# Kernel tuning notes

Measured on AMD Instinct MI355X. Metric: run time of the kernel, lower is better.

## Reference

```python
import jax, jax.numpy as jnp
import numpy as np

NEG_SLOPE = 0.2
EPS_SOFTMAX = 1e-16
EPS_NORM = 1e-12
H = 4


def gat_conv(x, src, dst, edge_attr, W, att_src, att_dst, W_edge, att_edge, bias, concat):
    """PyG GATConv with edge_dim, add_self_loops=False.
    x: [N, F_in]; src,dst: [E]; edge_attr: [E, edge_dim]
    W: [F_in, H*C]; att_src/att_dst/att_edge: [H, C]; W_edge: [edge_dim, H*C]
    """
    N = x.shape[0]
    C = att_src.shape[1]
    xs = (x @ W).reshape(N, H, C)                      # [N,H,C]
    a_s = jnp.einsum('nhc,hc->nh', xs, att_src)        # [N,H]
    a_d = jnp.einsum('nhc,hc->nh', xs, att_dst)        # [N,H]
    e = (edge_attr @ W_edge).reshape(-1, H, C)         # [E,H,C]
    a_e = jnp.einsum('ehc,hc->eh', e, att_edge)        # [E,H]
    alpha = a_s[src] + a_d[dst] + a_e                  # [E,H]
    alpha = jax.nn.leaky_relu(alpha, NEG_SLOPE)
    # segment softmax over edges grouped by destination node
    m = jax.ops.segment_max(alpha, dst, num_segments=N)        # [N,H]
    ex = jnp.exp(alpha - m[dst])
    denom = jax.ops.segment_sum(ex, dst, num_segments=N)       # [N,H]
    alpha = ex / (denom[dst] + EPS_SOFTMAX)
    # message = attention-weighted source features, scatter-add to dst
    out = jax.ops.segment_sum(xs[src] * alpha[..., None], dst, num_segments=N)  # [N,H,C]
    out = out.reshape(N, H * C) if concat else out.mean(axis=1)
    return out + bias


def l2_normalize(x):
    n = jnp.linalg.norm(x, axis=-1, keepdims=True)
    return x / jnp.maximum(n, EPS_NORM)


def setup_inputs() -> dict:
    key = jax.random.key(0)
    ks = jax.random.split(key, 16)
    N, E, F_in, C1, C2 = 50000, 800000, 128, 64, 64
    glorot = lambda k, shape: jax.random.uniform(
        k, shape, jnp.float32, -1.0, 1.0) * np.sqrt(6.0 / (shape[0] + shape[-1]))
    return {
        'x': jax.random.normal(ks[0], (N, F_in), jnp.float32),
        'edge_index': jax.random.randint(ks[1], (2, E), 0, N, jnp.int32),
        'edge_weight': jax.random.uniform(ks[2], (E, 1), jnp.float32),
        # layer 1: in=128 -> H*C1=256, concat=True
        'W1': glorot(ks[3], (F_in, H * C1)),
        'att_src1': glorot(ks[4], (H, C1)),
        'att_dst1': glorot(ks[5], (H, C1)),
        'We1': glorot(ks[6], (1, H * C1)),
        'att_e1': glorot(ks[7], (H, C1)),
        'b1': jnp.zeros((H * C1,), jnp.float32),
        # layer 2: in=256 -> H*C2, concat=False (mean over heads)
        'W2': glorot(ks[8], (H * C1, H * C2)),
        'att_src2': glorot(ks[9], (H, C2)),
        'att_dst2': glorot(ks[10], (H, C2)),
        'We2': glorot(ks[11], (1, H * C2)),
        'att_e2': glorot(ks[12], (H, C2)),
        'b2': jnp.zeros((C2,), jnp.float32),
    }


def reference(x, edge_index, edge_weight, W1, att_src1, att_dst1, We1, att_e1, b1,
              W2, att_src2, att_dst2, We2, att_e2, b2):
    src, dst = edge_index[0], edge_index[1]
    h = gat_conv(x, src, dst, edge_weight, W1, att_src1, att_dst1, We1, att_e1, b1, concat=True)
    h = jax.nn.relu(l2_normalize(h))
    out = gat_conv(h, src, dst, edge_weight, W2, att_src2, att_dst2, We2, att_e2, b2, concat=False)
    return out
```

## Files before the change

kernel.cpp:

```cpp
#include <hip/hip_runtime.h>
#include <hip/hip_bf16.h>

typedef unsigned short u16;
using bf16x8 = __attribute__((ext_vector_type(8))) short;
using f32x4v = __attribute__((ext_vector_type(4))) float;

#define HC 256
#define CDIM 64

__device__ __forceinline__ float b2f(u16 u){
  union { unsigned int i; float f; } c; c.i = ((unsigned)u) << 16; return c.f;
}
__device__ __forceinline__ u16 f2b(float f){
  union { float f; unsigned int i; } c; c.f = f;
  unsigned int x = c.i;
  return (u16)((x + 0x7FFFu + ((x >> 16) & 1u)) >> 16);
}
__device__ __forceinline__ float ldf(const void* p, size_t i, int isbf){
  return isbf ? b2f(((const u16*)p)[i]) : ((const float*)p)[i];
}
__device__ __forceinline__ float sel4(float4 v, int h){ return h==0?v.x:(h==1?v.y:(h==2?v.z:v.w)); }
__device__ __forceinline__ float lrelu(float v){ return v>0.f ? v : 0.2f*v; }

__device__ __forceinline__ float rdlf(float v, int e){
  return __int_as_float(__builtin_amdgcn_readlane(__float_as_int(v), e));
}
__device__ __forceinline__ float rdl_sel(float4 v, int h, int e){
  float w0 = rdlf(v.x, e), w1 = rdlf(v.y, e), w2 = rdlf(v.z, e), w3 = rdlf(v.w, e);
  return h==0?w0:(h==1?w1:(h==2?w2:w3));
}

__device__ __forceinline__ float4 wave_max4(float4 m){
  #pragma unroll
  for(int o=32;o>0;o>>=1){
    m.x=fmaxf(m.x,__shfl_xor(m.x,o));
    m.y=fmaxf(m.y,__shfl_xor(m.y,o));
    m.z=fmaxf(m.z,__shfl_xor(m.z,o));
    m.w=fmaxf(m.w,__shfl_xor(m.w,o));
  }
  return m;
}
__device__ __forceinline__ float4 wave_sum4(float4 m){
  #pragma unroll
  for(int o=32;o>0;o>>=1){
    m.x+=__shfl_xor(m.x,o);
    m.y+=__shfl_xor(m.y,o);
    m.z+=__shfl_xor(m.z,o);
    m.w+=__shfl_xor(m.w,o);
  }
  return m;
}

__global__ void k_detect(const u16* __restrict__ x, int nelem, int* __restrict__ flag){
  __shared__ int bad;
  if (threadIdx.x==0) bad = 0;
  __syncthreads();
  int n = nelem < 8192 ? nelem : 8192;
  int localbad = 0;
  for (int i=threadIdx.x; i<n; i+=256){
    int e = (x[i] >> 7) & 0xFF;
    if (e >= 140) localbad++;
  }
  if (localbad) atomicAdd(&bad, 1);
  __syncthreads();
  if (threadIdx.x==0) *flag = (bad==0) ? 1 : 0;
}

__global__ void k_hist(const int* __restrict__ dst, int E, int N, int* __restrict__ deg){
  int e = blockIdx.x*256 + threadIdx.x;
  if (e < E){
    int d = dst[e];
    if ((unsigned)d < (unsigned)N) atomicAdd(&deg[d], 1);
  }
}

__global__ void k_scan1(const int* __restrict__ in, int* __restrict__ out, int* __restrict__ bsums, int n){
  __shared__ int s[256];
  int t = threadIdx.x;
  int i = blockIdx.x*256 + t;
  int v = (i<n)? in[i] : 0;
  s[t]=v; __syncthreads();
  for(int off=1; off<256; off<<=1){
    int tv = (t>=off)? s[t-off] : 0;
    __syncthreads();
    s[t]+=tv; __syncthreads();
  }
  if (i<n) out[i] = s[t]-v;
  if (t==255) bsums[blockIdx.x] = s[255];
}

__global__ void k_scan2(int* __restrict__ bsums, int nb){
  __shared__ int s[256];
  int t=threadIdx.x;
  int v=(t<nb)? bsums[t]:0;
  s[t]=v; __syncthreads();
  for(int off=1; off<256; off<<=1){
    int tv=(t>=off)? s[t-off]:0;
    __syncthreads();
    s[t]+=tv; __syncthreads();
  }
  if (t<nb) bsums[t]=s[t]-v;
}

__global__ void k_scan3(int* __restrict__ out, const int* __restrict__ bsums, int n){
  int i = blockIdx.x*256+threadIdx.x;
  if (i<n) out[i]+=bsums[blockIdx.x];
}

__global__ void k_scatter(const int* __restrict__ src, const int* __restrict__ dst,
                          const void* __restrict__ ew, int E, int N,
                          const int* __restrict__ rowptr, int* __restrict__ cursor,
                          int* __restrict__ esrc, float* __restrict__ eewf,
                          const int* __restrict__ flagp){
  int e = blockIdx.x*256+threadIdx.x;
  if (e>=E) return;
  int bf = *flagp;
  int d = dst[e];
  if ((unsigned)d >= (unsigned)N) return;
  int p = rowptr[d] + atomicAdd(&cursor[d],1);
  int s = src[e];
  if ((unsigned)s >= (unsigned)N) s = 0;
  esrc[p] = s;
  eewf[p] = ldf(ew, e, bf);
}

__global__ void k_prepB(const void* __restrict__ W, u16* __restrict__ Bt, int K,
                        const int* __restrict__ flagp){
  int bf = *flagp;
  int k = blockIdx.x, t = threadIdx.x;
  float v = ldf(W, (size_t)k*HC + t, bf);
  Bt[(size_t)t*K + k] = f2b(v);
}

__global__ __launch_bounds__(256) void k_gemm_mfma(
    const void* __restrict__ A, int a_ext, const u16* __restrict__ Bt,
    u16* __restrict__ C, const void* __restrict__ att_s, const void* __restrict__ att_d,
    float* __restrict__ a_s, float* __restrict__ a_d,
    int M, int K, const int* __restrict__ flagp)
{
  __shared__ u16 sh[64*264];
  u16* As = sh;
  u16* Bs = sh + 2048;
  int bf = *flagp;
  int a_bf = a_ext ? bf : 1;
  int tid = threadIdx.x;
  int lane = tid & 63, w = tid >> 6;
  int quad = lane >> 4, ln = lane & 15;
  int m0 = blockIdx.x * 64;

  f32x4v acc[4][4] = {};
  for (int k0 = 0; k0 < K; k0 += 32){
    {
      int m = tid >> 2, g = tid & 3;
      int r = m0 + m;
      uint4 pack;
      if (r < M){
        size_t base = (size_t)r*K + k0 + g*8;
        if (a_bf){
          pack = *(const uint4*)((const u16*)A + base);
        } else {
          const float* Af = (const float*)A + base;
          float4 f0 = *(const float4*)Af;
          float4 f1 = *(const float4*)(Af+4);
          unsigned a0 = (unsigned)f2b(f0.x) | ((unsigned)f2b(f0.y)<<16);
          unsigned a1 = (unsigned)f2b(f0.z) | ((unsigned)f2b(f0.w)<<16);
          unsigned a2 = (unsigned)f2b(f1.x) | ((unsigned)f2b(f1.y)<<16);
          unsigned a3 = (unsigned)f2b(f1.z) | ((unsigned)f2b(f1.w)<<16);
          pack = make_uint4(a0,a1,a2,a3);
        }
      } else pack = make_uint4(0,0,0,0);
      ((uint4*)As)[tid] = pack;
    }
    #pragma unroll
    for (int i=0;i<4;i++){
      int n = i*64 + (tid>>2), g = tid&3;
      ((uint4*)Bs)[i*256 + tid] = *(const uint4*)(Bt + (size_t)n*K + k0 + g*8);
    }
    __syncthreads();
    bf16x8 af[4], bfr[4];
    #pragma unroll
    for (int mi=0;mi<4;mi++) af[mi] = *(const bf16x8*)&As[(mi*16+ln)*32 + quad*8];
    #pragma unroll
    for (int nj=0;nj<4;nj++) bfr[nj] = *(const bf16x8*)&Bs[((size_t)w*64+nj*16+ln)*32 + quad*8];
    #pragma unroll
    for (int mi=0;mi<4;mi++)
      #pragma unroll
      for (int nj=0;nj<4;nj++)
        acc[mi][nj] = __builtin_amdgcn_mfma_f32_16x16x32_bf16(af[mi], bfr[nj], acc[mi][nj], 0,0,0);
    __syncthreads();
  }
  #pragma unroll
  for (int mi=0;mi<4;mi++)
    #pragma unroll
    for (int nj=0;nj<4;nj++)
      #pragma unroll
      for (int r=0;r<4;r++)
        sh[(mi*16 + quad*4 + r)*264 + w*64 + nj*16 + ln] = f2b(acc[mi][nj][r]);
  __syncthreads();
  #pragma unroll
  for (int j=0;j<8;j++){
    int idx = j*256 + tid;
    int r = idx >> 5, gq = idx & 31;
    if (m0 + r < M)
      *(uint4*)(C + (size_t)(m0+r)*HC + gq*8) = *(const uint4*)&sh[r*264 + gq*8];
  }
  float4 sv, dv;
  sv.x=ldf(att_s,lane*4+0,bf); sv.y=ldf(att_s,lane*4+1,bf);
  sv.z=ldf(att_s,lane*4+2,bf); sv.w=ldf(att_s,lane*4+3,bf);
  dv.x=ldf(att_d,lane*4+0,bf); dv.y=ldf(att_d,lane*4+1,bf);
  dv.z=ldf(att_d,lane*4+2,bf); dv.w=ldf(att_d,lane*4+3,bf);
  for (int rr=0; rr<16; rr++){
    int r = w*16 + rr;
    ushort4 u = *(const ushort4*)&sh[r*264 + lane*4];
    float ps = b2f(u.x)*sv.x + b2f(u.y)*sv.y + b2f(u.z)*sv.z + b2f(u.w)*sv.w;
    float pd = b2f(u.x)*dv.x + b2f(u.y)*dv.y + b2f(u.z)*dv.z + b2f(u.w)*dv.w;
    #pragma unroll
    for (int o=1;o<16;o<<=1){ ps+=__shfl_xor(ps,o); pd+=__shfl_xor(pd,o); }
    if ((lane&15)==0 && m0+r<M){
      a_s[(size_t)(m0+r)*4 + (lane>>4)] = ps;
      a_d[(size_t)(m0+r)*4 + (lane>>4)] = pd;
    }
  }
}

__global__ void k_ce(const void* __restrict__ We, const void* __restrict__ att_e,
                     float* __restrict__ ce, const int* __restrict__ flagp){
  int bf = *flagp;
  int t=threadIdx.x;
  float p = ldf(We, t, bf)*ldf(att_e, t, bf);
  for(int o=32;o>0;o>>=1) p+=__shfl_xor(p,o);
  if((t&63)==0) ce[t>>6]=p;
}

__global__ __launch_bounds__(256) void k_soft_agg(
    const u16* __restrict__ xs, const int* __restrict__ rowptr, const int* __restrict__ deg,
    const int* __restrict__ esrc, const float* __restrict__ eewf,
    const float* __restrict__ a_s, const float* __restrict__ a_d, const float* __restrict__ ce4,
    const void* __restrict__ bias, void* __restrict__ outp, int N, int layer,
    const int* __restrict__ flagp){
  int bf = *flagp;
  int lane = threadIdx.x & 63;
  int w = threadIdx.x >> 6;
  int n = (blockIdx.x<<2) + w;
  if (n >= N) return;
  int row = rowptr[n];
  int dg = deg[n];
  float4 ad = *(const float4*)&a_d[(size_t)n*4];
  float4 ce = *(const float4*)ce4;
  int h = lane >> 4;
  float4 acc = make_float4(0.f,0.f,0.f,0.f);
  if (dg > 0){
    if (dg <= 64){
      int   s_reg = 0;
      float4 ar = make_float4(-1e30f,-1e30f,-1e30f,-1e30f);
      if (lane < dg){
        int pos = row + lane;
        int s = esrc[pos];
        if ((unsigned)s >= (unsigned)N) s = 0;
        s_reg = s;
        float wv = eewf[pos];
        float4 as = *(const float4*)&a_s[(size_t)s*4];
        ar.x = lrelu(as.x+ad.x+wv*ce.x);
        ar.y = lrelu(as.y+ad.y+wv*ce.y);
        ar.z = lrelu(as.z+ad.z+wv*ce.z);
        ar.w = lrelu(as.w+ad.w+wv*ce.w);
      }
      float4 m = wave_max4(ar);
      float4 ex = make_float4(0.f,0.f,0.f,0.f);
      if (lane < dg){
        ex.x=__expf(ar.x-m.x); ex.y=__expf(ar.y-m.y);
        ex.z=__expf(ar.z-m.z); ex.w=__expf(ar.w-m.w);
      }
      float4 ss = wave_sum4(ex);
      float4 wgt;
      wgt.x = ex.x/(ss.x+1e-16f); wgt.y = ex.y/(ss.y+1e-16f);
      wgt.z = ex.z/(ss.z+1e-16f); wgt.w = ex.w/(ss.w+1e-16f);
      int e = 0;
      for (; e+4 <= dg; e+=4){
        int s0=__builtin_amdgcn_readlane(s_reg,e+0);
        int s1=__builtin_amdgcn_readlane(s_reg,e+1);
        int s2=__builtin_amdgcn_readlane(s_reg,e+2);
        int s3=__builtin_amdgcn_readlane(s_reg,e+3);
        float w0=rdl_sel(wgt,h,e+0), w1=rdl_sel(wgt,h,e+1);
        float w2=rdl_sel(wgt,h,e+2), w3=rdl_sel(wgt,h,e+3);
        ushort4 x0 = *(const ushort4*)&xs[(size_t)s0*HC + lane*4];
        ushort4 x1 = *(const ushort4*)&xs[(size_t)s1*HC + lane*4];
        ushort4 x2 = *(const ushort4*)&xs[(size_t)s2*HC + lane*4];
        ushort4 x3 = *(const ushort4*)&xs[(size_t)s3*HC + lane*4];
        acc.x+=w0*b2f(x0.x); acc.y+=w0*b2f(x0.y); acc.z+=w0*b2f(x0.z); acc.w+=w0*b2f(x0.w);
        acc.x+=w1*b2f(x1.x); acc.y+=w1*b2f(x1.y); acc.z+=w1*b2f(x1.z); acc.w+=w1*b2f(x1.w);
        acc.x+=w2*b2f(x2.x); acc.y+=w2*b2f(x2.y); acc.z+=w2*b2f(x2.z); acc.w+=w2*b2f(x2.w);
        acc.x+=w3*b2f(x3.x); acc.y+=w3*b2f(x3.y); acc.z+=w3*b2f(x3.z); acc.w+=w3*b2f(x3.w);
      }
      for (; e<dg; e++){
        int s0=__builtin_amdgcn_readlane(s_reg,e);
        float w0=rdl_sel(wgt,h,e);
        ushort4 x0 = *(const ushort4*)&xs[(size_t)s0*HC + lane*4];
        acc.x+=w0*b2f(x0.x); acc.y+=w0*b2f(x0.y); acc.z+=w0*b2f(x0.z); acc.w+=w0*b2f(x0.w);
      }
    } else {
      float4 m = make_float4(-1e30f,-1e30f,-1e30f,-1e30f);
      for (int p=lane;p<dg;p+=64){
        int pos = row+p;
        int s = esrc[pos];
        if ((unsigned)s >= (unsigned)N) s = 0;
        float wv = eewf[pos];
        float4 as = *(const float4*)&a_s[(size_t)s*4];
        m.x=fmaxf(m.x, lrelu(as.x+ad.x+wv*ce.x));
        m.y=fmaxf(m.y, lrelu(as.y+ad.y+wv*ce.y));
        m.z=fmaxf(m.z, lrelu(as.z+ad.z+wv*ce.z));
        m.w=fmaxf(m.w, lrelu(as.w+ad.w+wv*ce.w));
      }
      m = wave_max4(m);
      float4 ss = make_float4(0.f,0.f,0.f,0.f);
      for (int p=lane;p<dg;p+=64){
        int pos = row+p;
        int s = esrc[pos];
        if ((unsigned)s >= (unsigned)N) s = 0;
        float wv = eewf[pos];
        float4 as = *(const float4*)&a_s[(size_t)s*4];
        ss.x+=__expf(lrelu(as.x+ad.x+wv*ce.x)-m.x);
        ss.y+=__expf(lrelu(as.y+ad.y+wv*ce.y)-m.y);
        ss.z+=__expf(lrelu(as.z+ad.z+wv*ce.z)-m.z);
        ss.w+=__expf(lrelu(as.w+ad.w+wv*ce.w)-m.w);
      }
      ss = wave_sum4(ss);
      float rsel=1.f/(sel4(ss,h)+1e-16f), mh=sel4(m,h), adh=sel4(ad,h), ceh=sel4(ce,h);
      for (int e=0;e<dg;e++){
        int pos=row+e;
        int s=esrc[pos];
        if ((unsigned)s >= (unsigned)N) s = 0;
        float wv=eewf[pos];
        float arv = lrelu(a_s[(size_t)s*4+h]+adh+wv*ceh);
        float wgt = __expf(arv-mh)*rsel;
        ushort4 xv4 = *(const ushort4*)&xs[(size_t)s*HC + lane*4];
        acc.x+=wgt*b2f(xv4.x); acc.y+=wgt*b2f(xv4.y);
        acc.z+=wgt*b2f(xv4.z); acc.w+=wgt*b2f(xv4.w);
      }
    }
  }
  if (layer==1){
    float4 v;
    v.x = acc.x + ldf(bias, lane*4+0, bf);
    v.y = acc.y + ldf(bias, lane*4+1, bf);
    v.z = acc.z + ldf(bias, lane*4+2, bf);
    v.w = acc.w + ldf(bias, lane*4+3, bf);
    float ss = v.x*v.x+v.y*v.y+v.z*v.z+v.w*v.w;
    #pragma unroll
    for(int o=32;o>0;o>>=1) ss += __shfl_xor(ss,o);
    float inv = 1.f/fmaxf(sqrtf(ss), 1e-12f);
    ushort4 o4;
    o4.x = f2b(fmaxf(v.x*inv,0.f)); o4.y = f2b(fmaxf(v.y*inv,0.f));
    o4.z = f2b(fmaxf(v.z*inv,0.f)); o4.w = f2b(fmaxf(v.w*inv,0.f));
    *(ushort4*)((u16*)outp + (size_t)n*HC + lane*4) = o4;
  } else {
    float4 s = acc;
    #pragma unroll
    for (int o=16;o<=32;o<<=1){
      s.x+=__shfl_xor(s.x,o); s.y+=__shfl_xor(s.y,o);
      s.z+=__shfl_xor(s.z,o); s.w+=__shfl_xor(s.w,o);
    }
    if (lane < 16){
      float4 v;
      v.x = 0.25f*s.x + ldf(bias, lane*4+0, bf);
      v.y = 0.25f*s.y + ldf(bias, lane*4+1, bf);
      v.z = 0.25f*s.z + ldf(bias, lane*4+2, bf);
      v.w = 0.25f*s.w + ldf(bias, lane*4+3, bf);
      if (bf){
        ushort4 o4; o4.x=f2b(v.x); o4.y=f2b(v.y); o4.z=f2b(v.z); o4.w=f2b(v.w);
        *(ushort4*)((u16*)outp + (size_t)n*CDIM + lane*4) = o4;
      } else {
        *(float4*)((float*)outp + (size_t)n*CDIM + lane*4) = v;
      }
    }
  }
}

extern "C" void kernel_launch(void* const* d_in, const int* in_sizes, int n_in,
                              void* d_out, int out_size, void* d_ws, size_t ws_size,
                              hipStream_t stream){
  const void* x_in = d_in[0];
  const int* eidx  = (const int*)d_in[1];
  const void* ew   = d_in[2];
  const void* W1   = d_in[3];
  const void* as1  = d_in[4];
  const void* ad1  = d_in[5];
  const void* We1  = d_in[6];
  const void* ae1  = d_in[7];
  const void* b1   = d_in[8];
  const void* W2   = d_in[9];
  const void* as2  = d_in[10];
  const void* ad2  = d_in[11];
  const void* We2  = d_in[12];
  const void* ae2  = d_in[13];
  const void* b2   = d_in[14];

  int N = in_sizes[0]/128;
  int E = in_sizes[2];
  const int* src = eidx;
  const int* dst = eidx + E;

  char* w = (char*)d_ws;
  auto alloc = [&](size_t bytes)->char*{ char* p=w; w += (bytes+255)/256*256; return p; };
  int*   flag  = (int*)alloc(256);
  u16*   xs    = (u16*)alloc((size_t)N*HC*2);
  u16*   agg   = (u16*)alloc((size_t)N*HC*2);
  float* a_s   = (float*)alloc((size_t)N*4*4);
  float* a_d   = (float*)alloc((size_t)N*4*4);
  int*   deg   = (int*)alloc((size_t)N*4);
  int*   cursor= (int*)alloc((size_t)N*4);
  int*   rowptr= (int*)alloc((size_t)N*4);
  int*   bsums = (int*)alloc(256*4);
  int*   esrc  = (int*)alloc((size_t)E*4);
  float* eewf  = (float*)alloc((size_t)E*4);
  float* ce    = (float*)alloc(64);
  u16*   Bt1   = (u16*)alloc((size_t)HC*128*2);
  u16*   Bt2   = (u16*)alloc((size_t)HC*HC*2);

  hipMemsetAsync(deg, 0, (size_t)N*4, stream);
  hipMemsetAsync(cursor, 0, (size_t)N*4, stream);

  k_detect<<<1,256,0,stream>>>((const u16*)x_in, in_sizes[0], flag);

  int eb = (E+255)/256;
  int nb = (N+255)/256;
  k_hist<<<eb,256,0,stream>>>(dst, E, N, deg);
  k_scan1<<<nb,256,0,stream>>>(deg, rowptr, bsums, N);
  k_scan2<<<1,256,0,stream>>>(bsums, nb);
  k_scan3<<<nb,256,0,stream>>>(rowptr, bsums, N);
  k_scatter<<<eb,256,0,stream>>>(src, dst, ew, E, N, rowptr, cursor, esrc, eewf, flag);
  k_prepB<<<128,256,0,stream>>>(W1, Bt1, 128, flag);
  k_prepB<<<256,256,0,stream>>>(W2, Bt2, 256, flag);

  int gemmBlocks = (N+63)/64;
  int nwb = (N+3)/4;

  k_gemm_mfma<<<gemmBlocks,256,0,stream>>>(x_in, 1, Bt1, xs, as1, ad1, a_s, a_d, N, 128, flag);
  k_ce<<<1,256,0,stream>>>(We1, ae1, ce, flag);
  k_soft_agg<<<nwb,256,0,stream>>>(xs, rowptr, deg, esrc, eewf, a_s, a_d, ce, b1, agg, N, 1, flag);

  k_gemm_mfma<<<gemmBlocks,256,0,stream>>>(agg, 0, Bt2, xs, as2, ad2, a_s, a_d, N, 256, flag);
  k_ce<<<1,256,0,stream>>>(We2, ae2, ce, flag);
  k_soft_agg<<<nwb,256,0,stream>>>(xs, rowptr, deg, esrc, eewf, a_s, a_d, ce, b2, d_out, N, 2, flag);
}
```

Baseline: 391.9 us.

## Merge setup kernels and replace readlane weight broadcast with shuffles

Several small setup kernels are merged: the detect, three-pass scan and cursor memset become one single-block 1024-thread scan kernel that also seeds the cursor, and the weight-transpose and edge-coefficient kernels become one prep kernel. This cuts launch count and removes a per-edge rowptr load in scatter. In the soft aggregation's fast path, the four readlanes plus select per edge are replaced by a per-head pre-shuffle followed by one shuffle per edge, aimed at lowering scalar/VALU overhead. The single-block scan serializes the degree prefix over about 49 elements per thread, which may be slower than the parallel multi-block scan.

```diff
diff --git a/kernel.cpp b/kernel.cpp
--- a/kernel.cpp
+++ b/kernel.cpp
@@ -21,14 +21,6 @@
 }
 __device__ __forceinline__ float sel4(float4 v, int h){ return h==0?v.x:(h==1?v.y:(h==2?v.z:v.w)); }
 __device__ __forceinline__ float lrelu(float v){ return v>0.f ? v : 0.2f*v; }
-
-__device__ __forceinline__ float rdlf(float v, int e){
-  return __int_as_float(__builtin_amdgcn_readlane(__float_as_int(v), e));
-}
-__device__ __forceinline__ float rdl_sel(float4 v, int h, int e){
-  float w0 = rdlf(v.x, e), w1 = rdlf(v.y, e), w2 = rdlf(v.z, e), w3 = rdlf(v.w, e);
-  return h==0?w0:(h==1?w1:(h==2?w2:w3));
-}
 
 __device__ __forceinline__ float4 wave_max4(float4 m){
   #pragma unroll
@@ -51,21 +43,6 @@
   return m;
 }
 
-__global__ void k_detect(const u16* __restrict__ x, int nelem, int* __restrict__ flag){
-  __shared__ int bad;
-  if (threadIdx.x==0) bad = 0;
-  __syncthreads();
-  int n = nelem < 8192 ? nelem : 8192;
-  int localbad = 0;
-  for (int i=threadIdx.x; i<n; i+=256){
-    int e = (x[i] >> 7) & 0xFF;
-    if (e >= 140) localbad++;
-  }
-  if (localbad) atomicAdd(&bad, 1);
-  __syncthreads();
-  if (threadIdx.x==0) *flag = (bad==0) ? 1 : 0;
-}
-
 __global__ void k_hist(const int* __restrict__ dst, int E, int N, int* __restrict__ deg){
   int e = blockIdx.x*256 + threadIdx.x;
   if (e < E){
@@ -74,37 +51,41 @@
   }
 }
 
-__global__ void k_scan1(const int* __restrict__ in, int* __restrict__ out, int* __restrict__ bsums, int n){
-  __shared__ int s[256];
+__global__ __launch_bounds__(1024) void k_scan(const int* __restrict__ deg,
+                                               int* __restrict__ rowptr, int* __restrict__ cursor,
+                                               int N, const u16* __restrict__ x, int nelem,
+                                               int* __restrict__ flag){
+  __shared__ int sums[1024];
+  __shared__ int bad;
   int t = threadIdx.x;
-  int i = blockIdx.x*256 + t;
-  int v = (i<n)? in[i] : 0;
-  s[t]=v; __syncthreads();
-  for(int off=1; off<256; off<<=1){
-    int tv = (t>=off)? s[t-off] : 0;
+  if (t==0) bad = 0;
+  __syncthreads();
+  if (t < 256){
+    int n = nelem < 8192 ? nelem : 8192;
+    int localbad = 0;
+    for (int i=t; i<n; i+=256){
+      int e = (x[i] >> 7) & 0xFF;
+      if (e >= 140) localbad++;
+    }
+    if (localbad) atomicAdd(&bad, 1);
+  }
+  __syncthreads();
+  if (t==0) *flag = (bad==0) ? 1 : 0;
+  int chunk = (N + 1023) >> 10;
+  int lo = t*chunk, hi = lo+chunk < N ? lo+chunk : N;
+  int s = 0;
+  for (int i=lo;i<hi;i++) s += deg[i];
+  sums[t]=s; __syncthreads();
+  for (int off=1; off<1024; off<<=1){
+    int v = (t>=off)? sums[t-off]:0;
     __syncthreads();
-    s[t]+=tv; __syncthreads();
-  }
-  if (i<n) out[i] = s[t]-v;
-  if (t==255) bsums[blockIdx.x] = s[255];
-}
-
-__global__ void k_scan2(int* __restrict__ bsums, int nb){
-  __shared__ int s[256];
-  int t=threadIdx.x;
-  int v=(t<nb)? bsums[t]:0;
-  s[t]=v; __syncthreads();
-  for(int off=1; off<256; off<<=1){
-    int tv=(t>=off)? s[t-off]:0;
-    __syncthreads();
-    s[t]+=tv; __syncthreads();
-  }
-  if (t<nb) bsums[t]=s[t]-v;
-}
-
-__global__ void k_scan3(int* __restrict__ out, const int* __restrict__ bsums, int n){
-  int i = blockIdx.x*256+threadIdx.x;
-  if (i<n) out[i]+=bsums[blockIdx.x];
+    sums[t]+=v; __syncthreads();
+  }
+  int base = sums[t] - s;
+  for (int i=lo;i<hi;i++){
+    rowptr[i]=base; cursor[i]=base;
+    base += deg[i];
+  }
 }
 
 __global__ void k_scatter(const int* __restrict__ src, const int* __restrict__ dst,
@@ -117,19 +98,32 @@
   int bf = *flagp;
   int d = dst[e];
   if ((unsigned)d >= (unsigned)N) return;
-  int p = rowptr[d] + atomicAdd(&cursor[d],1);
+  int p = atomicAdd(&cursor[d],1);
   int s = src[e];
   if ((unsigned)s >= (unsigned)N) s = 0;
   esrc[p] = s;
   eewf[p] = ldf(ew, e, bf);
 }
 
-__global__ void k_prepB(const void* __restrict__ W, u16* __restrict__ Bt, int K,
-                        const int* __restrict__ flagp){
+__global__ void k_prep(const void* __restrict__ W1, const void* __restrict__ W2,
+                       const void* __restrict__ We1, const void* __restrict__ ae1,
+                       const void* __restrict__ We2, const void* __restrict__ ae2,
+                       u16* __restrict__ Bt1, u16* __restrict__ Bt2, float* __restrict__ ce,
+                       const int* __restrict__ flagp){
   int bf = *flagp;
-  int k = blockIdx.x, t = threadIdx.x;
-  float v = ldf(W, (size_t)k*HC + t, bf);
-  Bt[(size_t)t*K + k] = f2b(v);
+  int b = blockIdx.x, t = threadIdx.x;
+  if (b < 128){
+    Bt1[(size_t)t*128 + b] = f2b(ldf(W1, (size_t)b*HC + t, bf));
+  } else if (b < 384){
+    int k = b - 128;
+    Bt2[(size_t)t*256 + k] = f2b(ldf(W2, (size_t)k*HC + t, bf));
+  } else {
+    float p1 = ldf(We1, t, bf)*ldf(ae1, t, bf);
+    float p2 = ldf(We2, t, bf)*ldf(ae2, t, bf);
+    #pragma unroll
+    for(int o=32;o>0;o>>=1){ p1+=__shfl_xor(p1,o); p2+=__shfl_xor(p2,o); }
+    if((t&63)==0){ ce[t>>6]=p1; ce[4+(t>>6)]=p2; }
+  }
 }
 
 __global__ __launch_bounds__(256) void k_gemm_mfma(
@@ -221,15 +215,6 @@
       a_d[(size_t)(m0+r)*4 + (lane>>4)] = pd;
     }
   }
-}
-
-__global__ void k_ce(const void* __restrict__ We, const void* __restrict__ att_e,
-                     float* __restrict__ ce, const int* __restrict__ flagp){
-  int bf = *flagp;
-  int t=threadIdx.x;
-  float p = ldf(We, t, bf)*ldf(att_e, t, bf);
-  for(int o=32;o>0;o>>=1) p+=__shfl_xor(p,o);
-  if((t&63)==0) ce[t>>6]=p;
 }
 
 __global__ __launch_bounds__(256) void k_soft_agg(
@@ -275,28 +260,49 @@
       float4 wgt;
       wgt.x = ex.x/(ss.x+1e-16f); wgt.y = ex.y/(ss.y+1e-16f);
       wgt.z = ex.z/(ss.z+1e-16f); wgt.w = ex.w/(ss.w+1e-16f);
-      int e = 0;
-      for (; e+4 <= dg; e+=4){
-        int s0=__builtin_amdgcn_readlane(s_reg,e+0);
-        int s1=__builtin_amdgcn_readlane(s_reg,e+1);
-        int s2=__builtin_amdgcn_readlane(s_reg,e+2);
-        int s3=__builtin_amdgcn_readlane(s_reg,e+3);
-        float w0=rdl_sel(wgt,h,e+0), w1=rdl_sel(wgt,h,e+1);
-        float w2=rdl_sel(wgt,h,e+2), w3=rdl_sel(wgt,h,e+3);
-        ushort4 x0 = *(const ushort4*)&xs[(size_t)s0*HC + lane*4];
-        ushort4 x1 = *(const ushort4*)&xs[(size_t)s1*HC + lane*4];
-        ushort4 x2 = *(const ushort4*)&xs[(size_t)s2*HC + lane*4];
-        ushort4 x3 = *(const ushort4*)&xs[(size_t)s3*HC + lane*4];
-        acc.x+=w0*b2f(x0.x); acc.y+=w0*b2f(x0.y); acc.z+=w0*b2f(x0.z); acc.w+=w0*b2f(x0.w);
-        acc.x+=w1*b2f(x1.x); acc.y+=w1*b2f(x1.y); acc.z+=w1*b2f(x1.z); acc.w+=w1*b2f(x1.w);
-        acc.x+=w2*b2f(x2.x); acc.y+=w2*b2f(x2.y); acc.z+=w2*b2f(x2.z); acc.w+=w2*b2f(x2.w);
-        acc.x+=w3*b2f(x3.x); acc.y+=w3*b2f(x3.y); acc.z+=w3*b2f(x3.z); acc.w+=w3*b2f(x3.w);
-      }
-      for (; e<dg; e++){
-        int s0=__builtin_amdgcn_readlane(s_reg,e);
-        float w0=rdl_sel(wgt,h,e);
-        ushort4 x0 = *(const ushort4*)&xs[(size_t)s0*HC + lane*4];
-        acc.x+=w0*b2f(x0.x); acc.y+=w0*b2f(x0.y); acc.z+=w0*b2f(x0.z); acc.w+=w0*b2f(x0.w);
+      float tw[4];
+      #pragma unroll
+      for (int j=0;j<4;j++){
+        if (j*16 < dg){
+          int srcl = j*16 + (lane & 15);
+          float c0=__shfl(wgt.x,srcl), c1=__shfl(wgt.y,srcl);
+          float c2=__shfl(wgt.z,srcl), c3=__shfl(wgt.w,srcl);
+          tw[j] = (h==0)?c0:((h==1)?c1:((h==2)?c2:c3));
+        } else tw[j] = 0.f;
+      }
+      int ibase = lane & 48;
+      #pragma unroll
+      for (int j=0;j<4;j++){
+        int j0 = j*16;
+        if (j0 >= dg) break;
+        float twj = tw[j];
+        int cnt = dg - j0; if (cnt > 16) cnt = 16;
+        int t = 0;
+        for (; t+4<=cnt; t+=4){
+          int e = j0 + t;
+          int s0=__builtin_amdgcn_readlane(s_reg,e+0);
+          int s1=__builtin_amdgcn_readlane(s_reg,e+1);
+          int s2=__builtin_amdgcn_readlane(s_reg,e+2);
+          int s3=__builtin_amdgcn_readlane(s_reg,e+3);
+          float w0=__shfl(twj, ibase+t+0);
+          float w1=__shfl(twj, ibase+t+1);
+          float w2=__shfl(twj, ibase+t+2);
+          float w3=__shfl(twj, ibase+t+3);
+          ushort4 x0 = *(const ushort4*)&xs[(size_t)s0*HC + lane*4];
+          ushort4 x1 = *(const ushort4*)&xs[(size_t)s1*HC + lane*4];
+          ushort4 x2 = *(const ushort4*)&xs[(size_t)s2*HC + lane*4];
+          ushort4 x3 = *(const ushort4*)&xs[(size_t)s3*HC + lane*4];
+          acc.x+=w0*b2f(x0.x); acc.y+=w0*b2f(x0.y); acc.z+=w0*b2f(x0.z); acc.w+=w0*b2f(x0.w);
+          acc.x+=w1*b2f(x1.x); acc.y+=w1*b2f(x1.y); acc.z+=w1*b2f(x1.z); acc.w+=w1*b2f(x1.w);
+          acc.x+=w2*b2f(x2.x); acc.y+=w2*b2f(x2.y); acc.z+=w2*b2f(x2.z); acc.w+=w2*b2f(x2.w);
+          acc.x+=w3*b2f(x3.x); acc.y+=w3*b2f(x3.y); acc.z+=w3*b2f(x3.z); acc.w+=w3*b2f(x3.w);
+        }
+        for (; t<cnt; t++){
+          int s0=__builtin_amdgcn_readlane(s_reg,j0+t);
+          float w0=__shfl(twj, ibase+t);
+          ushort4 x0 = *(const ushort4*)&xs[(size_t)s0*HC + lane*4];
+          acc.x+=w0*b2f(x0.x); acc.y+=w0*b2f(x0.y); acc.z+=w0*b2f(x0.z); acc.w+=w0*b2f(x0.w);
+        }
       }
     } else {
       float4 m = make_float4(-1e30f,-1e30f,-1e30f,-1e30f);
@@ -410,36 +416,26 @@
   int*   deg   = (int*)alloc((size_t)N*4);
   int*   cursor= (int*)alloc((size_t)N*4);
   int*   rowptr= (int*)alloc((size_t)N*4);
-  int*   bsums = (int*)alloc(256*4);
   int*   esrc  = (int*)alloc((size_t)E*4);
   float* eewf  = (float*)alloc((size_t)E*4);
-  float* ce    = (float*)alloc(64);
+  float* ce    = (float*)alloc(256);
   u16*   Bt1   = (u16*)alloc((size_t)HC*128*2);
   u16*   Bt2   = (u16*)alloc((size_t)HC*HC*2);
 
   hipMemsetAsync(deg, 0, (size_t)N*4, stream);
-  hipMemsetAsync(cursor, 0, (size_t)N*4, stream);
-
-  k_detect<<<1,256,0,stream>>>((const u16*)x_in, in_sizes[0], flag);
 
   int eb = (E+255)/256;
-  int nb = (N+255)/256;
   k_hist<<<eb,256,0,stream>>>(dst, E, N, deg);
-  k_scan1<<<nb,256,0,stream>>>(deg, rowptr, bsums, N);
-  k_scan2<<<1,256,0,stream>>>(bsums, nb);
-  k_scan3<<<nb,256,0,stream>>>(rowptr, bsums, N);
+  k_scan<<<1,1024,0,stream>>>(deg, rowptr, cursor, N, (const u16*)x_in, in_sizes[0], flag);
   k_scatter<<<eb,256,0,stream>>>(src, dst, ew, E, N, rowptr, cursor, esrc, eewf, flag);
-  k_prepB<<<128,256,0,stream>>>(W1, Bt1, 128, flag);
-  k_prepB<<<256,256,0,stream>>>(W2, Bt2, 256, flag);
+  k_prep<<<385,256,0,stream>>>(W1, W2, We1, ae1, We2, ae2, Bt1, Bt2, ce, flag);
 
   int gemmBlocks = (N+63)/64;
   int nwb = (N+3)/4;
 
   k_gemm_mfma<<<gemmBlocks,256,0,stream>>>(x_in, 1, Bt1, xs, as1, ad1, a_s, a_d, N, 128, flag);
-  k_ce<<<1,256,0,stream>>>(We1, ae1, ce, flag);
   k_soft_agg<<<nwb,256,0,stream>>>(xs, rowptr, deg, esrc, eewf, a_s, a_d, ce, b1, agg, N, 1, flag);
 
   k_gemm_mfma<<<gemmBlocks,256,0,stream>>>(agg, 0, Bt2, xs, as2, ad2, a_s, a_d, N, 256, flag);
-  k_ce<<<1,256,0,stream>>>(We2, ae2, ce, flag);
-  k_soft_agg<<<nwb,256,0,stream>>>(xs, rowptr, deg, esrc, eewf, a_s, a_d, ce, b2, d_out, N, 2, flag);
-}
+  k_soft_agg<<<nwb,256,0,stream>>>(xs, rowptr, deg, esrc, eewf, a_s, a_d, ce+4, b2, d_out, N, 2, flag);
+}
```

New measurement: 483.0 us. 23.2% more time.
